# Kernel tuning notes

Measured on AMD Instinct MI355X. Metric: run time of the kernel, lower is better.

The kernel has to match this reference:

```python
import jax, jax.numpy as jnp
import numpy as np

N = 50000   # nodes
E = 800000  # edges (before self-loops)
IN = 128; H = 4; C = 32; HC = H * C; OUT = 47
EPS = 1e-16  # PyG softmax denominator eps
NEG_SLOPE = 0.2


def setup_inputs() -> dict:
    key = jax.random.key(0)
    ks = jax.random.split(key, 20)
    g = lambda k, shape, s=0.1: (jax.random.normal(k, shape, dtype=jnp.float32) * s)
    inp = {}
    inp["x"] = jax.random.normal(ks[0], (N, IN), dtype=jnp.float32)
    inp["edge_index"] = jax.random.randint(ks[1], (2, E), 0, N, dtype=jnp.int32)
    # layer 0: GATConv(IN -> H*C, concat=True) + skip Linear(IN -> HC)
    inp["lin_w0"] = g(ks[2], (IN, HC)); inp["att_src0"] = g(ks[3], (H, C)); inp["att_dst0"] = g(ks[4], (H, C))
    inp["bias0"] = g(ks[5], (HC,)); inp["skip_w0"] = g(ks[6], (IN, HC)); inp["skip_b0"] = g(ks[7], (HC,))
    # layer 1: GATConv(HC -> H*C, concat=True) + skip Linear(HC -> HC)
    inp["lin_w1"] = g(ks[8], (HC, HC)); inp["att_src1"] = g(ks[9], (H, C)); inp["att_dst1"] = g(ks[10], (H, C))
    inp["bias1"] = g(ks[11], (HC,)); inp["skip_w1"] = g(ks[12], (HC, HC)); inp["skip_b1"] = g(ks[13], (HC,))
    # layer 2: GATConv(HC -> OUT, heads=H, concat=False) + skip Linear(HC -> OUT)
    inp["lin_w2"] = g(ks[14], (HC, H * OUT)); inp["att_src2"] = g(ks[15], (H, OUT)); inp["att_dst2"] = g(ks[16], (H, OUT))
    inp["bias2"] = g(ks[17], (OUT,)); inp["skip_w2"] = g(ks[18], (HC, OUT)); inp["skip_b2"] = g(ks[19], (OUT,))
    return inp


def _gat_conv(x, src, dst, lin_w, att_src, att_dst, bias, concat):
    """PyG GATConv (self-loops already appended to src/dst)."""
    h, c = att_src.shape
    n = x.shape[0]
    xh = (x @ lin_w).reshape(n, h, c)                      # [N, H, C]
    a_src = jnp.einsum('nhc,hc->nh', xh, att_src)          # [N, H]
    a_dst = jnp.einsum('nhc,hc->nh', xh, att_dst)          # [N, H]
    e = a_src[src] + a_dst[dst]                            # [E', H]
    e = jax.nn.leaky_relu(e, NEG_SLOPE)
    # segment softmax over incoming edges per destination node
    m = jax.ops.segment_max(e, dst, num_segments=n)        # [N, H]
    ex = jnp.exp(e - m[dst])
    s = jax.ops.segment_sum(ex, dst, num_segments=n)       # [N, H]
    alpha = ex / (s[dst] + EPS)                            # [E', H]
    out = jax.ops.segment_sum(xh[src] * alpha[:, :, None], dst, num_segments=n)  # [N, H, C]
    out = out.reshape(n, h * c) if concat else out.mean(axis=1)
    return out + bias


def reference(x, edge_index, lin_w0, att_src0, att_dst0, bias0, skip_w0, skip_b0,
              lin_w1, att_src1, att_dst1, bias1, skip_w1, skip_b1,
              lin_w2, att_src2, att_dst2, bias2, skip_w2, skip_b2):
    n = x.shape[0]
    loop = jnp.arange(n, dtype=edge_index.dtype)
    src = jnp.concatenate([edge_index[0], loop])
    dst = jnp.concatenate([edge_index[1], loop])
    # layer 0 (+ skip, ELU; dropout is identity at inference)
    x = _gat_conv(x, src, dst, lin_w0, att_src0, att_dst0, bias0, True) + x @ skip_w0 + skip_b0
    x = jax.nn.elu(x)
    # layer 1
    x = _gat_conv(x, src, dst, lin_w1, att_src1, att_dst1, bias1, True) + x @ skip_w1 + skip_b1
    x = jax.nn.elu(x)
    # layer 2 (concat=False -> head mean), no activation
    x = _gat_conv(x, src, dst, lin_w2, att_src2, att_dst2, bias2, False) + x @ skip_w2 + skip_b2
    return x
```

## Files before the change

### kernel.cpp

```cpp
#include <hip/hip_runtime.h>
#include <math.h>
#include <type_traits>

#define KD 128
#define HC 128
#define NF2 188
#define NF2PB 192
#define OUTC 47

typedef __attribute__((ext_vector_type(8))) __bf16 bf16x8;
typedef __attribute__((ext_vector_type(4))) float f32x4;
typedef __attribute__((ext_vector_type(2))) float f32x2;

#ifdef __has_builtin
#if __has_builtin(__builtin_amdgcn_cvt_pk_f32_fp8)
#define HAVE_CVT_FP8_DEC 1
#endif
#if __has_builtin(__builtin_amdgcn_cvt_pk_fp8_f32)
#define HAVE_CVT_FP8_ENC 1
#endif
#endif

__device__ inline float bfhi_to_f(unsigned int u) {
    union { unsigned int u; float f; } c; c.u = u & 0xFFFF0000u; return c.f;
}
__device__ inline float bflo_to_f(unsigned int u) {
    union { unsigned int u; float f; } c; c.u = u << 16; return c.f;
}
__device__ inline unsigned short f_to_bfu(float f) {
    return __builtin_bit_cast(unsigned short, (__bf16)f);
}
__device__ inline unsigned int pk_bf(float a, float b) {
    return (unsigned int)f_to_bfu(a) | ((unsigned int)f_to_bfu(b) << 16);
}

__device__ inline void dot2bf(float& acc, unsigned int x, unsigned int a) {
    asm("v_dot2_f32_bf16 %0, %1, %2, %0" : "+v"(acc) : "v"(x), "v"(a));
}
__device__ inline unsigned int permb(unsigned int hi, unsigned int lo, unsigned int sel) {
    return __builtin_amdgcn_perm(hi, lo, sel);
}

#ifndef HAVE_CVT_FP8_DEC
__device__ inline float fp8_to_f32_b(unsigned int b) {
    int e = (b >> 3) & 15, m = b & 7;
    float v = e ? ldexpf((float)(8 + m), e - 10) : ldexpf((float)m, -9);
    return (b & 0x80) ? -v : v;
}
#endif
__device__ inline void fp8x4_dec(unsigned int q, float& a, float& b, float& c, float& d) {
#ifdef HAVE_CVT_FP8_DEC
    f32x2 lo = __builtin_amdgcn_cvt_pk_f32_fp8((int)q, false);
    f32x2 hi = __builtin_amdgcn_cvt_pk_f32_fp8((int)q, true);
    a = lo[0]; b = lo[1]; c = hi[0]; d = hi[1];
#else
    a = fp8_to_f32_b(q & 0xFF); b = fp8_to_f32_b((q >> 8) & 0xFF);
    c = fp8_to_f32_b((q >> 16) & 0xFF); d = fp8_to_f32_b((q >> 24) & 0xFF);
#endif
}
__device__ inline unsigned char f32_to_fp8(float v) {
#ifdef HAVE_CVT_FP8_ENC
    return (unsigned char)(__builtin_amdgcn_cvt_pk_fp8_f32(v, v, 0, false) & 0xFF);
#else
    unsigned u = __builtin_bit_cast(unsigned, v);
    unsigned s = (u >> 24) & 0x80;
    float a = fabsf(v);
    if (a < 0.0009765625f) return (unsigned char)s;
    if (a >= 448.f) return (unsigned char)(s | 0x7E);
    int e; float m = frexpf(a, &e);
    int E = e - 1 + 7;
    int mi = (int)rintf(m * 16.f);
    if (mi == 16) { mi = 8; ++E; if (E >= 16) return (unsigned char)(s | 0x7E); }
    if (E <= 0) {
        int q = (int)rintf(a * 512.f); if (q > 7) q = 7;
        return (unsigned char)(s | q);
    }
    return (unsigned char)(s | (E << 3) | (mi - 8));
#endif
}
__device__ inline float fp8dot(unsigned int q, float4 al, float acc) {
    float a, b, c, d;
    fp8x4_dec(q, a, b, c, d);
    return acc + al.x * a + al.y * b + al.z * c + al.w * d;
}

__global__ void count_kernel(const int* __restrict__ dst, int* deg, int e) {
    int t = blockIdx.x * blockDim.x + threadIdx.x;
    int base = t * 8;
    if (base + 7 < e) {
        int4 d0 = *(const int4*)(dst + base);
        int4 d1 = *(const int4*)(dst + base + 4);
        atomicAdd(&deg[d0.x], 1); atomicAdd(&deg[d0.y], 1);
        atomicAdd(&deg[d0.z], 1); atomicAdd(&deg[d0.w], 1);
        atomicAdd(&deg[d1.x], 1); atomicAdd(&deg[d1.y], 1);
        atomicAdd(&deg[d1.z], 1); atomicAdd(&deg[d1.w], 1);
    } else {
        for (int k = base; k < e; ++k) atomicAdd(&deg[dst[k]], 1);
    }
}

__global__ __launch_bounds__(256) void scan_base_kernel(
    int* __restrict__ deg, int* counter,
    int* __restrict__ row_ptr, int* __restrict__ fill, int* __restrict__ col, int n) {
    int i = blockIdx.x * 256 + threadIdx.x;
    int v = (i < n) ? (deg[i] + 1) : 0;
    int lane = threadIdx.x & 63, w = threadIdx.x >> 6;
    int incl = v;
#pragma unroll
    for (int off = 1; off < 64; off <<= 1) {
        int u = __shfl_up(incl, off, 64);
        if (lane >= off) incl += u;
    }
    __shared__ int wsum[4];
    __shared__ int base_sh;
    if (lane == 63) wsum[w] = incl;
    __syncthreads();
    if (threadIdx.x == 0)
        base_sh = atomicAdd(counter, wsum[0] + wsum[1] + wsum[2] + wsum[3]);
    int woff = 0;
    for (int k = 0; k < w; ++k) woff += wsum[k];
    __syncthreads();
    int excl = base_sh + woff + incl - v;
    if (i < n) {
        row_ptr[i] = excl;
        col[excl] = i;
        fill[i] = excl + 1;
        deg[i] = v;
    }
}

__global__ void fill_kernel(const int* __restrict__ ei, int* fill, int* col, int e) {
    int t = blockIdx.x * blockDim.x + threadIdx.x;
    int base = t * 8;
    if (base + 7 < e) {
        int4 s0 = *(const int4*)(ei + base);
        int4 s1 = *(const int4*)(ei + base + 4);
        int4 d0 = *(const int4*)(ei + e + base);
        int4 d1 = *(const int4*)(ei + e + base + 4);
        int p0 = atomicAdd(&fill[d0.x], 1);
        int p1 = atomicAdd(&fill[d0.y], 1);
        int p2 = atomicAdd(&fill[d0.z], 1);
        int p3 = atomicAdd(&fill[d0.w], 1);
        int p4 = atomicAdd(&fill[d1.x], 1);
        int p5 = atomicAdd(&fill[d1.y], 1);
        int p6 = atomicAdd(&fill[d1.z], 1);
        int p7 = atomicAdd(&fill[d1.w], 1);
        col[p0] = s0.x; col[p1] = s0.y; col[p2] = s0.z; col[p3] = s0.w;
        col[p4] = s1.x; col[p5] = s1.y; col[p6] = s1.z; col[p7] = s1.w;
    } else {
        for (int k = base; k < e; ++k) {
            int pos = atomicAdd(&fill[ei[e + k]], 1);
            col[pos] = ei[k];
        }
    }
}

__global__ __launch_bounds__(256) void prep_w_kernel(
    const float* __restrict__ lw0, const float* __restrict__ sw0,
    const float* __restrict__ lw1, const float* __restrict__ sw1,
    const float* __restrict__ lw2, const float* __restrict__ sw2,
    __bf16* __restrict__ bt) {
    int idx = blockIdx.x * 256 + threadIdx.x;
    int buf = idx >> 15;
    int r = idx & 32767;
    int n = r >> 7, k = r & 127;
    float v = 0.f;
    if (buf == 0) v = (n < 128) ? lw0[k * 128 + n] : sw0[k * 128 + n - 128];
    else if (buf == 1) v = (n < 128) ? lw1[k * 128 + n] : sw1[k * 128 + n - 128];
    else {
        if (n < 188) v = lw2[k * 188 + n];
        else if (n >= 192 && n < 239) v = sw2[k * 47 + n - 192];
    }
    bt[idx] = (__bf16)v;
}

template <typename AT, typename SKT, int NLIN, int NSK, int TR>
__global__ __launch_bounds__(256) void gemm_fused_kernel(
    const AT* __restrict__ A, const __bf16* __restrict__ Bt,
    void* __restrict__ out0, int N0, int ldc0,
    const float* __restrict__ bias1, SKT* __restrict__ out1, int N1, int M) {
    __shared__ __bf16 As[64][136];
    int tid = threadIdx.x;
    int m0 = blockIdx.x * 64;

#pragma unroll
    for (int rep = 0; rep < 4; ++rep) {
        int idx = tid + rep * 256;
        int row = idx >> 4, seg = idx & 15;
        int gm = m0 + row;
        bf16x8 v = {};
        if (gm < M) {
            if constexpr (std::is_same<AT, float>::value) {
                const float* p = A + gm * KD + seg * 8;
                float4 f0 = *(const float4*)p;
                float4 f1 = *(const float4*)(p + 4);
                v[0] = (__bf16)f0.x; v[1] = (__bf16)f0.y; v[2] = (__bf16)f0.z; v[3] = (__bf16)f0.w;
                v[4] = (__bf16)f1.x; v[5] = (__bf16)f1.y; v[6] = (__bf16)f1.z; v[7] = (__bf16)f1.w;
            } else {
                v = *(const bf16x8*)(A + gm * KD + seg * 8);
            }
        }
        *(bf16x8*)&As[row][seg * 8] = v;
    }
    __syncthreads();

    int w = tid >> 6, lane = tid & 63;
    int lr = lane & 15, quad = lane >> 4;

#pragma unroll
    for (int t = 0; t < NLIN + NSK; ++t) {
        bool second = t >= NLIN;
        int N = second ? N1 : N0;
        int n0 = (second ? (t - NLIN) : t) * 64;
        const __bf16* bbase = Bt + ((t * 64 + lr) << 7) + quad * 8;

        f32x4 acc[4] = {};
#pragma unroll
        for (int kc = 0; kc < 128; kc += 32) {
            bf16x8 a0 = *(const bf16x8*)&As[w * 16 + lr][kc + quad * 8];
            bf16x8 b0 = *(const bf16x8*)(bbase + kc);
            bf16x8 b1 = *(const bf16x8*)(bbase + (16 << 7) + kc);
            bf16x8 b2 = *(const bf16x8*)(bbase + (32 << 7) + kc);
            bf16x8 b3 = *(const bf16x8*)(bbase + (48 << 7) + kc);
            acc[0] = __builtin_amdgcn_mfma_f32_16x16x32_bf16(a0, b0, acc[0], 0, 0, 0);
            acc[1] = __builtin_amdgcn_mfma_f32_16x16x32_bf16(a0, b1, acc[1], 0, 0, 0);
            acc[2] = __builtin_amdgcn_mfma_f32_16x16x32_bf16(a0, b2, acc[2], 0, 0, 0);
            acc[3] = __builtin_amdgcn_mfma_f32_16x16x32_bf16(a0, b3, acc[3], 0, 0, 0);
        }
#pragma unroll
        for (int c = 0; c < 4; ++c) {
#pragma unroll
            for (int reg = 0; reg < 4; ++reg) {
                int row = m0 + w * 16 + quad * 4 + reg;
                int colg = n0 + c * 16 + lr;
                if (row < M && colg < N) {
                    float v = acc[c][reg];
                    if (second) {
                        v += bias1[colg];
                        out1[row * N + colg] = (SKT)v;
                    } else if (TR) {
                        int h = (colg * 1395) >> 16;
                        ((unsigned char*)out0)[row * ldc0 + (colg - 47 * h) * 4 + h] =
                            f32_to_fp8(v);
                    } else {
                        ((__bf16*)out0)[row * ldc0 + colg] = (__bf16)v;
                    }
                }
            }
        }
    }
}

__global__ __launch_bounds__(256) void att_kernel(
    const __bf16* __restrict__ xh, const float* __restrict__ att_s,
    const float* __restrict__ att_d, float* __restrict__ a_src,
    float* __restrict__ a_dst, int n) {
    int tid = blockIdx.x * 256 + threadIdx.x;
    int node = tid >> 4;
    int l16 = threadIdx.x & 15;
    if (node >= n) return;
    uint4 q = ((const uint4*)xh)[node * 16 + l16];
    int f0 = l16 * 8;
    float4 as0 = *(const float4*)(att_s + f0);
    float4 as1 = *(const float4*)(att_s + f0 + 4);
    float4 ad0 = *(const float4*)(att_d + f0);
    float4 ad1 = *(const float4*)(att_d + f0 + 4);
    float x0 = bflo_to_f(q.x), x1 = bfhi_to_f(q.x);
    float x2 = bflo_to_f(q.y), x3 = bfhi_to_f(q.y);
    float x4 = bflo_to_f(q.z), x5 = bfhi_to_f(q.z);
    float x6 = bflo_to_f(q.w), x7 = bfhi_to_f(q.w);
    float hs = x0 * as0.x + x1 * as0.y + x2 * as0.z + x3 * as0.w
             + x4 * as1.x + x5 * as1.y + x6 * as1.z + x7 * as1.w;
    float hd = x0 * ad0.x + x1 * ad0.y + x2 * ad0.z + x3 * ad0.w
             + x4 * ad1.x + x5 * ad1.y + x6 * ad1.z + x7 * ad1.w;
    hs += __shfl_xor(hs, 1, 64); hs += __shfl_xor(hs, 2, 64);
    hd += __shfl_xor(hd, 1, 64); hd += __shfl_xor(hd, 2, 64);
    if ((l16 & 3) == 0) {
        int h = l16 >> 2;
        a_src[node * 4 + h] = hs;
        a_dst[node * 4 + h] = hd;
    }
}

__global__ __launch_bounds__(256) void att2_kernel(
    const unsigned char* __restrict__ xh8, const float* __restrict__ att_s,
    const float* __restrict__ att_d, float* __restrict__ a_src,
    float* __restrict__ a_dst, int n) {
    int node = (blockIdx.x * 256 + threadIdx.x) >> 6;
    int lane = threadIdx.x & 63;
    if (node >= n) return;
    float ps0 = 0.f, ps1 = 0.f, ps2 = 0.f, ps3 = 0.f;
    float pd0 = 0.f, pd1 = 0.f, pd2 = 0.f, pd3 = 0.f;
    if (lane < 47) {
        unsigned int q = ((const unsigned int*)(xh8 + node * NF2PB))[lane];
        float x0, x1, x2, x3;
        fp8x4_dec(q, x0, x1, x2, x3);
        ps0 = x0 * att_s[lane];       ps1 = x1 * att_s[47 + lane];
        ps2 = x2 * att_s[94 + lane];  ps3 = x3 * att_s[141 + lane];
        pd0 = x0 * att_d[lane];       pd1 = x1 * att_d[47 + lane];
        pd2 = x2 * att_d[94 + lane];  pd3 = x3 * att_d[141 + lane];
    }
#pragma unroll
    for (int off = 1; off <= 32; off <<= 1) {
        ps0 += __shfl_xor(ps0, off, 64); ps1 += __shfl_xor(ps1, off, 64);
        ps2 += __shfl_xor(ps2, off, 64); ps3 += __shfl_xor(ps3, off, 64);
        pd0 += __shfl_xor(pd0, off, 64); pd1 += __shfl_xor(pd1, off, 64);
        pd2 += __shfl_xor(pd2, off, 64); pd3 += __shfl_xor(pd3, off, 64);
    }
    if (lane < 4) {
        float vs = (lane == 0) ? ps0 : (lane == 1) ? ps1 : (lane == 2) ? ps2 : ps3;
        float vd = (lane == 0) ? pd0 : (lane == 1) ? pd1 : (lane == 2) ? pd2 : pd3;
        a_src[node * 4 + lane] = vs;
        a_dst[node * 4 + lane] = vd;
    }
}

template <int MODE>
__global__ __launch_bounds__(256) void agg_kernel(
    const void* __restrict__ xhp, const float* __restrict__ a_src,
    const float* __restrict__ a_dst, const void* __restrict__ skipp,
    const float* __restrict__ bias, const int* __restrict__ row_ptr,
    const int* __restrict__ deg, const int* __restrict__ col,
    void* __restrict__ outp, int n) {
    __shared__ float s_af[4][64][4];
    __shared__ unsigned s_ap[4][32][4];
    __shared__ int s_j[4][64];
    int w = threadIdx.x >> 6;
    int lane = threadIdx.x & 63;
    int node = (blockIdx.x << 2) + w;
    bool active = node < n;
    int node_c = active ? node : 0;
    int start = row_ptr[node_c];
    int end = start + (active ? deg[node_c] : 0);
    float4 ad4 = *(const float4*)(a_dst + 4 * node_c);
    float adh[4] = {ad4.x, ad4.y, ad4.z, ad4.w};

    int e0 = start + lane;
    bool ok0 = e0 < end;
    int jcap = ok0 ? col[e0] : 0;
    float evc[4];
    {
        float4 as4 = *(const float4*)(a_src + 4 * jcap);
        float v0 = as4.x + adh[0]; v0 = v0 > 0.f ? v0 : 0.2f * v0;
        float v1 = as4.y + adh[1]; v1 = v1 > 0.f ? v1 : 0.2f * v1;
        float v2 = as4.z + adh[2]; v2 = v2 > 0.f ? v2 : 0.2f * v2;
        float v3 = as4.w + adh[3]; v3 = v3 > 0.f ? v3 : 0.2f * v3;
        evc[0] = ok0 ? __expf(v0) : 0.f;
        evc[1] = ok0 ? __expf(v1) : 0.f;
        evc[2] = ok0 ? __expf(v2) : 0.f;
        evc[3] = ok0 ? __expf(v3) : 0.f;
    }
    float s[4] = {evc[0], evc[1], evc[2], evc[3]};
    for (int e = e0 + 64; e < end; e += 64) {
        int j = col[e];
        float4 as4 = *(const float4*)(a_src + 4 * j);
        float ev[4] = {as4.x + adh[0], as4.y + adh[1], as4.z + adh[2], as4.w + adh[3]};
#pragma unroll
        for (int h = 0; h < 4; ++h) {
            float v = ev[h] > 0.f ? ev[h] : 0.2f * ev[h];
            s[h] += __expf(v);
        }
    }
#pragma unroll
    for (int off = 32; off >= 1; off >>= 1)
#pragma unroll
        for (int h = 0; h < 4; ++h) s[h] += __shfl_xor(s[h], off, 64);
    float inv[4];
#pragma unroll
    for (int h = 0; h < 4; ++h) inv[h] = 1.f / (s[h] + 1e-16f);

    int half = lane >> 5, fl = lane & 31, myh2 = fl >> 3;
    bool lv = lane < 47;
    float acc0 = 0.f, acc1 = 0.f, acc2 = 0.f, acc3 = 0.f;
    const uint2* xb2 = (const uint2*)xhp;
    const unsigned int* x8 = (const unsigned int*)xhp;

    auto run_chunk = [&](int cnt) {
        if constexpr (MODE == 0) {
            int npair = (cnt + 1) >> 1;
            int p = half;
            for (; p + 2 < npair; p += 4) {
                int2 j0 = *(const int2*)&s_j[w][2 * p];
                int2 j1 = *(const int2*)&s_j[w][2 * p + 4];
                unsigned ap0 = s_ap[w][p][myh2];
                unsigned ap1 = s_ap[w][p + 2][myh2];
                uint2 qa0 = xb2[(j0.x << 5) + fl];
                uint2 qb0 = xb2[(j0.y << 5) + fl];
                uint2 qa1 = xb2[(j1.x << 5) + fl];
                uint2 qb1 = xb2[(j1.y << 5) + fl];
                dot2bf(acc0, permb(qb0.x, qa0.x, 0x05040100u), ap0);
                dot2bf(acc1, permb(qb0.x, qa0.x, 0x07060302u), ap0);
                dot2bf(acc2, permb(qb0.y, qa0.y, 0x05040100u), ap0);
                dot2bf(acc3, permb(qb0.y, qa0.y, 0x07060302u), ap0);
                dot2bf(acc0, permb(qb1.x, qa1.x, 0x05040100u), ap1);
                dot2bf(acc1, permb(qb1.x, qa1.x, 0x07060302u), ap1);
                dot2bf(acc2, permb(qb1.y, qa1.y, 0x05040100u), ap1);
                dot2bf(acc3, permb(qb1.y, qa1.y, 0x07060302u), ap1);
            }
            for (; p < npair; p += 2) {
                int2 j0 = *(const int2*)&s_j[w][2 * p];
                unsigned ap0 = s_ap[w][p][myh2];
                uint2 qa0 = xb2[(j0.x << 5) + fl];
                uint2 qb0 = xb2[(j0.y << 5) + fl];
                dot2bf(acc0, permb(qb0.x, qa0.x, 0x05040100u), ap0);
                dot2bf(acc1, permb(qb0.x, qa0.x, 0x07060302u), ap0);
                dot2bf(acc2, permb(qb0.y, qa0.y, 0x05040100u), ap0);
                dot2bf(acc3, permb(qb0.y, qa0.y, 0x07060302u), ap0);
            }
        } else {
            int t = 0;
            for (; t + 7 < cnt; t += 8) {
                unsigned int q0 = lv ? x8[s_j[w][t] * 48 + lane] : 0u;
                unsigned int q1 = lv ? x8[s_j[w][t + 1] * 48 + lane] : 0u;
                unsigned int q2 = lv ? x8[s_j[w][t + 2] * 48 + lane] : 0u;
                unsigned int q3 = lv ? x8[s_j[w][t + 3] * 48 + lane] : 0u;
                unsigned int q4 = lv ? x8[s_j[w][t + 4] * 48 + lane] : 0u;
                unsigned int q5 = lv ? x8[s_j[w][t + 5] * 48 + lane] : 0u;
                unsigned int q6 = lv ? x8[s_j[w][t + 6] * 48 + lane] : 0u;
                unsigned int q7 = lv ? x8[s_j[w][t + 7] * 48 + lane] : 0u;
                acc0 = fp8dot(q0, *(const float4*)&s_af[w][t][0], acc0);
                acc0 = fp8dot(q1, *(const float4*)&s_af[w][t + 1][0], acc0);
                acc0 = fp8dot(q2, *(const float4*)&s_af[w][t + 2][0], acc0);
                acc0 = fp8dot(q3, *(const float4*)&s_af[w][t + 3][0], acc0);
                acc0 = fp8dot(q4, *(const float4*)&s_af[w][t + 4][0], acc0);
                acc0 = fp8dot(q5, *(const float4*)&s_af[w][t + 5][0], acc0);
                acc0 = fp8dot(q6, *(const float4*)&s_af[w][t + 6][0], acc0);
                acc0 = fp8dot(q7, *(const float4*)&s_af[w][t + 7][0], acc0);
            }
            for (; t + 3 < cnt; t += 4) {
                unsigned int q0 = lv ? x8[s_j[w][t] * 48 + lane] : 0u;
                unsigned int q1 = lv ? x8[s_j[w][t + 1] * 48 + lane] : 0u;
                unsigned int q2 = lv ? x8[s_j[w][t + 2] * 48 + lane] : 0u;
                unsigned int q3 = lv ? x8[s_j[w][t + 3] * 48 + lane] : 0u;
                acc0 = fp8dot(q0, *(const float4*)&s_af[w][t][0], acc0);
                acc0 = fp8dot(q1, *(const float4*)&s_af[w][t + 1][0], acc0);
                acc0 = fp8dot(q2, *(const float4*)&s_af[w][t + 2][0], acc0);
                acc0 = fp8dot(q3, *(const float4*)&s_af[w][t + 3][0], acc0);
            }
            for (; t < cnt; ++t) {
                unsigned int q = lv ? x8[s_j[w][t] * 48 + lane] : 0u;
                acc0 = fp8dot(q, *(const float4*)&s_af[w][t][0], acc0);
            }
        }
    };

    {
        float al[4];
#pragma unroll
        for (int h = 0; h < 4; ++h) al[h] = evc[h] * inv[h];
        s_j[w][lane] = jcap;
        if constexpr (MODE == 0) {
            float o0 = __shfl_xor(al[0], 1, 64);
            float o1 = __shfl_xor(al[1], 1, 64);
            float o2 = __shfl_xor(al[2], 1, 64);
            float o3 = __shfl_xor(al[3], 1, 64);
            if (!(lane & 1)) {
                uint4 pk = make_uint4(pk_bf(al[0], o0), pk_bf(al[1], o1),
                                      pk_bf(al[2], o2), pk_bf(al[3], o3));
                *(uint4*)&s_ap[w][lane >> 1][0] = pk;
            }
        } else {
            *(float4*)&s_af[w][lane][0] = make_float4(al[0], al[1], al[2], al[3]);
        }
        int cnt = end - start; if (cnt > 64) cnt = 64;
        run_chunk(cnt);
    }
    for (int base = start + 64; base < end; base += 64) {
        int e = base + lane;
        bool ok = e < end;
        int jv = ok ? col[e] : 0;
        float4 as4 = *(const float4*)(a_src + 4 * jv);
        float asv[4] = {as4.x, as4.y, as4.z, as4.w};
        float al[4];
#pragma unroll
        for (int h = 0; h < 4; ++h) {
            float ev = asv[h] + adh[h];
            ev = ev > 0.f ? ev : 0.2f * ev;
            al[h] = ok ? __expf(ev) * inv[h] : 0.f;
        }
        s_j[w][lane] = jv;
        if constexpr (MODE == 0) {
            float o0 = __shfl_xor(al[0], 1, 64);
            float o1 = __shfl_xor(al[1], 1, 64);
            float o2 = __shfl_xor(al[2], 1, 64);
            float o3 = __shfl_xor(al[3], 1, 64);
            if (!(lane & 1)) {
                uint4 pk = make_uint4(pk_bf(al[0], o0), pk_bf(al[1], o1),
                                      pk_bf(al[2], o2), pk_bf(al[3], o3));
                *(uint4*)&s_ap[w][lane >> 1][0] = pk;
            }
        } else {
            *(float4*)&s_af[w][lane][0] = make_float4(al[0], al[1], al[2], al[3]);
        }
        int cnt = end - base; if (cnt > 64) cnt = 64;
        run_chunk(cnt);
    }

    if constexpr (MODE == 0) {
        acc0 += __shfl_xor(acc0, 32, 64);
        acc1 += __shfl_xor(acc1, 32, 64);
        acc2 += __shfl_xor(acc2, 32, 64);
        acc3 += __shfl_xor(acc3, 32, 64);
        if (active && half == 0) {
            float4 bb = *(const float4*)(bias + 4 * fl);
            uint2 skq = ((const uint2*)skipp)[(node << 5) + fl];
            float v0 = acc0 + bb.x + bflo_to_f(skq.x);
            float v1 = acc1 + bb.y + bfhi_to_f(skq.x);
            float v2 = acc2 + bb.z + bflo_to_f(skq.y);
            float v3 = acc3 + bb.w + bfhi_to_f(skq.y);
            v0 = v0 > 0.f ? v0 : (__expf(v0) - 1.f);
            v1 = v1 > 0.f ? v1 : (__expf(v1) - 1.f);
            v2 = v2 > 0.f ? v2 : (__expf(v2) - 1.f);
            v3 = v3 > 0.f ? v3 : (__expf(v3) - 1.f);
            uint2 o = make_uint2(pk_bf(v0, v1), pk_bf(v2, v3));
            ((uint2*)outp)[(node << 5) + fl] = o;
        }
    } else {
        if (active && lane < OUTC) {
            const float* skip = (const float*)skipp;
            float v = acc0 * 0.25f + bias[lane] + skip[node * OUTC + lane];
            ((float*)outp)[node * OUTC + lane] = v;
        }
    }
}

extern "C" void kernel_launch(void* const* d_in, const int* in_sizes, int n_in,
                              void* d_out, int out_size, void* d_ws, size_t ws_size,
                              hipStream_t stream) {
    const float* x        = (const float*)d_in[0];
    const int*   ei       = (const int*)d_in[1];
    const float* lin_w0   = (const float*)d_in[2];
    const float* att_src0 = (const float*)d_in[3];
    const float* att_dst0 = (const float*)d_in[4];
    const float* bias0    = (const float*)d_in[5];
    const float* skip_w0  = (const float*)d_in[6];
    const float* skip_b0  = (const float*)d_in[7];
    const float* lin_w1   = (const float*)d_in[8];
    const float* att_src1 = (const float*)d_in[9];
    const float* att_dst1 = (const float*)d_in[10];
    const float* bias1    = (const float*)d_in[11];
    const float* skip_w1  = (const float*)d_in[12];
    const float* skip_b1  = (const float*)d_in[13];
    const float* lin_w2   = (const float*)d_in[14];
    const float* att_src2 = (const float*)d_in[15];
    const float* att_dst2 = (const float*)d_in[16];
    const float* bias2    = (const float*)d_in[17];
    const float* skip_w2  = (const float*)d_in[18];
    const float* skip_b2  = (const float*)d_in[19];
    float* out = (float*)d_out;

    const int N = in_sizes[0] / KD;
    const int E = in_sizes[1] / 2;
    const int ET_ = E + N;

    char* ws = (char*)d_ws;
    size_t off = 0;
    auto alloc = [&](size_t bytes) -> void* {
        void* p = ws + off;
        off = (off + bytes + 255) & ~(size_t)255;
        return p;
    };
    void*   xh      = alloc((size_t)N * HC * 2 + 256);
    __bf16* buf_bf  = (__bf16*)alloc((size_t)N * HC * 2);
    void*   skipbuf = alloc((size_t)N * HC * 4);
    float* a_src    = (float*)alloc((size_t)N * 4 * 4);
    float* a_dst    = (float*)alloc((size_t)N * 4 * 4);
    int* deg        = (int*)alloc((size_t)N * 4);
    int* row_ptr    = (int*)alloc((size_t)N * 4);
    int* fill       = (int*)alloc((size_t)N * 4);
    int* col        = (int*)alloc((size_t)ET_ * 4);
    int* counter    = (int*)alloc(256);
    __bf16* Bt      = (__bf16*)alloc((size_t)3 * 256 * 128 * 2);

    prep_w_kernel<<<384, 256, 0, stream>>>(lin_w0, skip_w0, lin_w1, skip_w1,
                                           lin_w2, skip_w2, Bt);

    hipMemsetAsync(deg, 0, (size_t)N * 4, stream);
    hipMemsetAsync(counter, 0, 4, stream);
    count_kernel<<<(E / 8 + 255) / 256, 256, 0, stream>>>(ei + E, deg, E);
    scan_base_kernel<<<(N + 255) / 256, 256, 0, stream>>>(deg, counter, row_ptr, fill, col, N);
    fill_kernel<<<(E / 8 + 255) / 256, 256, 0, stream>>>(ei, fill, col, E);

    dim3 blk(256);
    int mblocks = (N + 63) / 64;
    int wave_blocks = (N + 3) / 4;
    int att_blocks = (N * 16 + 255) / 256;

    gemm_fused_kernel<float, __bf16, 2, 2, 0><<<mblocks, blk, 0, stream>>>(
        x, Bt, xh, HC, HC, skip_b0, (__bf16*)skipbuf, HC, N);
    att_kernel<<<att_blocks, blk, 0, stream>>>((const __bf16*)xh, att_src0, att_dst0,
                                               a_src, a_dst, N);
    agg_kernel<0><<<wave_blocks, blk, 0, stream>>>(xh, a_src, a_dst, skipbuf, bias0,
                                                   row_ptr, deg, col, buf_bf, N);
    gemm_fused_kernel<__bf16, __bf16, 2, 2, 0><<<mblocks, blk, 0, stream>>>(
        buf_bf, Bt + 32768, xh, HC, HC, skip_b1, (__bf16*)skipbuf, HC, N);
    att_kernel<<<att_blocks, blk, 0, stream>>>((const __bf16*)xh, att_src1, att_dst1,
                                               a_src, a_dst, N);
    agg_kernel<0><<<wave_blocks, blk, 0, stream>>>(xh, a_src, a_dst, skipbuf, bias1,
                                                   row_ptr, deg, col, buf_bf, N);
    gemm_fused_kernel<__bf16, float, 3, 1, 1><<<mblocks, blk, 0, stream>>>(
        buf_bf, Bt + 65536, xh, NF2, NF2PB, skip_b2, (float*)skipbuf, OUTC, N);
    att2_kernel<<<wave_blocks, blk, 0, stream>>>((const unsigned char*)xh, att_src2,
                                                 att_dst2, a_src, a_dst, N);
    agg_kernel<1><<<wave_blocks, blk, 0, stream>>>(xh, a_src, a_dst, skipbuf, bias2,
                                                   row_ptr, deg, col, out, N);
}
```

Before: 456.5 us.

## Stage GEMM weight tiles in LDS and shrink per-thread work in CSR build

The fused GEMM now copies each 64x128 weight tile into shared memory before the MFMA loop, instead of every wave reading B fragments straight from global memory. This adds two barriers per tile. The count and fill kernels handle 2 edges per thread instead of 8, which launches 4x more threads so more atomics are in flight. The scattered col writes in fill now use nontemporal stores to avoid polluting the cache.

```diff
diff --git a/kernel.cpp b/kernel.cpp
--- a/kernel.cpp
+++ b/kernel.cpp
@@ -86,14 +86,10 @@
 
 __global__ void count_kernel(const int* __restrict__ dst, int* deg, int e) {
     int t = blockIdx.x * blockDim.x + threadIdx.x;
-    int base = t * 8;
-    if (base + 7 < e) {
-        int4 d0 = *(const int4*)(dst + base);
-        int4 d1 = *(const int4*)(dst + base + 4);
-        atomicAdd(&deg[d0.x], 1); atomicAdd(&deg[d0.y], 1);
-        atomicAdd(&deg[d0.z], 1); atomicAdd(&deg[d0.w], 1);
-        atomicAdd(&deg[d1.x], 1); atomicAdd(&deg[d1.y], 1);
-        atomicAdd(&deg[d1.z], 1); atomicAdd(&deg[d1.w], 1);
+    int base = t * 2;
+    if (base + 1 < e) {
+        int2 d = *(const int2*)(dst + base);
+        atomicAdd(&deg[d.x], 1); atomicAdd(&deg[d.y], 1);
     } else {
         for (int k = base; k < e; ++k) atomicAdd(&deg[dst[k]], 1);
     }
@@ -131,26 +127,18 @@
 
 __global__ void fill_kernel(const int* __restrict__ ei, int* fill, int* col, int e) {
     int t = blockIdx.x * blockDim.x + threadIdx.x;
-    int base = t * 8;
-    if (base + 7 < e) {
-        int4 s0 = *(const int4*)(ei + base);
-        int4 s1 = *(const int4*)(ei + base + 4);
-        int4 d0 = *(const int4*)(ei + e + base);
-        int4 d1 = *(const int4*)(ei + e + base + 4);
-        int p0 = atomicAdd(&fill[d0.x], 1);
-        int p1 = atomicAdd(&fill[d0.y], 1);
-        int p2 = atomicAdd(&fill[d0.z], 1);
-        int p3 = atomicAdd(&fill[d0.w], 1);
-        int p4 = atomicAdd(&fill[d1.x], 1);
-        int p5 = atomicAdd(&fill[d1.y], 1);
-        int p6 = atomicAdd(&fill[d1.z], 1);
-        int p7 = atomicAdd(&fill[d1.w], 1);
-        col[p0] = s0.x; col[p1] = s0.y; col[p2] = s0.z; col[p3] = s0.w;
-        col[p4] = s1.x; col[p5] = s1.y; col[p6] = s1.z; col[p7] = s1.w;
+    int base = t * 2;
+    if (base + 1 < e) {
+        int2 s = *(const int2*)(ei + base);
+        int2 d = *(const int2*)(ei + e + base);
+        int p0 = atomicAdd(&fill[d.x], 1);
+        int p1 = atomicAdd(&fill[d.y], 1);
+        __builtin_nontemporal_store(s.x, &col[p0]);
+        __builtin_nontemporal_store(s.y, &col[p1]);
     } else {
         for (int k = base; k < e; ++k) {
             int pos = atomicAdd(&fill[ei[e + k]], 1);
-            col[pos] = ei[k];
+            __builtin_nontemporal_store(ei[k], &col[pos]);
         }
     }
 }
@@ -180,6 +168,7 @@
     void* __restrict__ out0, int N0, int ldc0,
     const float* __restrict__ bias1, SKT* __restrict__ out1, int N1, int M) {
     __shared__ __bf16 As[64][136];
+    __shared__ __bf16 Bs[64][136];
     int tid = threadIdx.x;
     int m0 = blockIdx.x * 64;
 
@@ -212,16 +201,24 @@
         bool second = t >= NLIN;
         int N = second ? N1 : N0;
         int n0 = (second ? (t - NLIN) : t) * 64;
-        const __bf16* bbase = Bt + ((t * 64 + lr) << 7) + quad * 8;
+        if (t) __syncthreads();
+#pragma unroll
+        for (int rep = 0; rep < 4; ++rep) {
+            int idx = tid + rep * 256;
+            int row = idx >> 4, seg = idx & 15;
+            *(bf16x8*)&Bs[row][seg * 8] =
+                *(const bf16x8*)(Bt + ((t * 64 + row) << 7) + seg * 8);
+        }
+        __syncthreads();
 
         f32x4 acc[4] = {};
 #pragma unroll
         for (int kc = 0; kc < 128; kc += 32) {
             bf16x8 a0 = *(const bf16x8*)&As[w * 16 + lr][kc + quad * 8];
-            bf16x8 b0 = *(const bf16x8*)(bbase + kc);
-            bf16x8 b1 = *(const bf16x8*)(bbase + (16 << 7) + kc);
-            bf16x8 b2 = *(const bf16x8*)(bbase + (32 << 7) + kc);
-            bf16x8 b3 = *(const bf16x8*)(bbase + (48 << 7) + kc);
+            bf16x8 b0 = *(const bf16x8*)&Bs[lr][kc + quad * 8];
+            bf16x8 b1 = *(const bf16x8*)&Bs[16 + lr][kc + quad * 8];
+            bf16x8 b2 = *(const bf16x8*)&Bs[32 + lr][kc + quad * 8];
+            bf16x8 b3 = *(const bf16x8*)&Bs[48 + lr][kc + quad * 8];
             acc[0] = __builtin_amdgcn_mfma_f32_16x16x32_bf16(a0, b0, acc[0], 0, 0, 0);
             acc[1] = __builtin_amdgcn_mfma_f32_16x16x32_bf16(a0, b1, acc[1], 0, 0, 0);
             acc[2] = __builtin_amdgcn_mfma_f32_16x16x32_bf16(a0, b2, acc[2], 0, 0, 0);
@@ -577,9 +574,9 @@
 
     hipMemsetAsync(deg, 0, (size_t)N * 4, stream);
     hipMemsetAsync(counter, 0, 4, stream);
-    count_kernel<<<(E / 8 + 255) / 256, 256, 0, stream>>>(ei + E, deg, E);
+    count_kernel<<<(E / 2 + 255) / 256, 256, 0, stream>>>(ei + E, deg, E);
     scan_base_kernel<<<(N + 255) / 256, 256, 0, stream>>>(deg, counter, row_ptr, fill, col, N);
-    fill_kernel<<<(E / 8 + 255) / 256, 256, 0, stream>>>(ei, fill, col, E);
+    fill_kernel<<<(E / 2 + 255) / 256, 256, 0, stream>>>(ei, fill, col, E);
 
     dim3 blk(256);
     int mblocks = (N + 63) / 64;
```

Result: faster. 409.8 us (-10.2%).
